# Optimization experiments

Hardware: AMD Instinct MI355X
Metric: run time of the kernel (lower is better)

Reference implementation:

```python
import jax, jax.numpy as jnp
import numpy as np

TOP_K = 6  # heapq.nlargest(6, ...) in the original

N_USERS_ROWS = 8192
EMB_DIM = 512
NUM_USER_IDS = 8192
NUM_ITEMS = 4096


def setup_inputs() -> dict:
    key = jax.random.key(0)
    k1, k2, k3, k4 = jax.random.split(key, 4)
    users_embeddings = jax.random.normal(k1, (N_USERS_ROWS, EMB_DIM), dtype=jnp.float32)
    n_users = jax.random.randint(k2, (N_USERS_ROWS,), 0, NUM_USER_IDS, dtype=jnp.int64)
    n_entitys = jax.random.randint(k3, (N_USERS_ROWS,), 0, NUM_ITEMS, dtype=jnp.int64)
    # 0/1 membership matrix standing in for the `course` dict: user_id -> set of items
    interactions = jax.random.randint(k4, (NUM_USER_IDS, NUM_ITEMS), 0, 2, dtype=jnp.int32)
    return {
        "users_embeddings": users_embeddings,
        "n_users": n_users,
        "n_entitys": n_entitys,
        "interactions": interactions,
    }


def reference(users_embeddings, n_users, n_entitys, interactions):
    # Pairwise cosine similarity: normalize rows, one GEMM.  [N, N]
    norms = jnp.linalg.norm(users_embeddings, axis=-1, keepdims=True)
    xn = users_embeddings / norms
    sim = jnp.einsum("nd,md->nm", xn, xn)
    # top-6 most similar users per row (includes self, like the original)
    top_vals, top_idx = jax.lax.top_k(sim, TOP_K)  # [N, 6] each
    # choice(course=n_entitys[l], user=n_users[idx]) -> 0/1 membership gather
    neighbor_user_ids = n_users[top_idx]            # [N, 6]
    memb = interactions[neighbor_user_ids, n_entitys[:, None]]  # [N, 6] int
    # p[l] = sum_k sim(l, idx_k) * memb / 6
    user_choice_degree = jnp.sum(top_vals * memb.astype(top_vals.dtype), axis=-1) / 6.0
    return user_choice_degree
```

## Files before the change

kernel.cpp:

```cpp
#include <hip/hip_runtime.h>
#include <math.h>

typedef unsigned char  uchar_t;
typedef unsigned int   uint32;
typedef __attribute__((ext_vector_type(4)))  int   i32x4;
typedef __attribute__((ext_vector_type(8)))  int   i32x8;
typedef __attribute__((ext_vector_type(16))) float f32x16;

#define EMB     512
#define NROWS   8192
#define NITEMS  4096
#define NSPLIT  16
#define CPS     512
#define CTILE   128
#define QTILE   128
#define NSTEPS  32
#define LDEPTH  8
#define KEEP    8
#define NRESC   16

#define GLOAD_LDS(gp, lp) __builtin_amdgcn_global_load_lds( \
    (const __attribute__((address_space(1))) void*)(gp),    \
    (__attribute__((address_space(3))) void*)(lp), 16, 0, 0)

__device__ inline uint32 packkey(float v, int idx) {
    uint32 u = __float_as_uint(v);
    uint32 s = u ^ ((u & 0x80000000u) ? 0xFFFFFFFFu : 0x80000000u);
    return (s & 0xFFFFE000u) | ((uint32)idx ^ 0x1FFFu);
}

__global__ void prep_kernel(const float* __restrict__ E,
                            uchar_t* __restrict__ Xq, double* __restrict__ invd) {
    const int row  = blockIdx.x * 4 + (threadIdx.x >> 6);
    const int lane = threadIdx.x & 63;
    const float4* p = (const float4*)(E + (size_t)row * EMB);
    float4 f0 = p[lane];
    float4 f1 = p[lane + 64];
    double s = (double)f0.x*f0.x + (double)f0.y*f0.y + (double)f0.z*f0.z + (double)f0.w*f0.w
             + (double)f1.x*f1.x + (double)f1.y*f1.y + (double)f1.z*f1.z + (double)f1.w*f1.w;
#pragma unroll
    for (int m = 32; m > 0; m >>= 1) s += __shfl_xor(s, m);
    const double inv = 1.0 / sqrt(s);
    if (lane == 0) invd[row] = inv;
    const float sc = (float)inv * 16.0f;
    int w0 = 0, w1 = 0;
    w0 = __builtin_amdgcn_cvt_pk_fp8_f32(f0.x * sc, f0.y * sc, w0, false);
    w0 = __builtin_amdgcn_cvt_pk_fp8_f32(f0.z * sc, f0.w * sc, w0, true);
    w1 = __builtin_amdgcn_cvt_pk_fp8_f32(f1.x * sc, f1.y * sc, w1, false);
    w1 = __builtin_amdgcn_cvt_pk_fp8_f32(f1.z * sc, f1.w * sc, w1, true);
    ((int2*)(Xq + (size_t)row * EMB))[lane] = make_int2(w0, w1);
}

__global__ __launch_bounds__(256, 4) void sim_topk_mfma(
    const uchar_t* __restrict__ Xq, uint32* __restrict__ keys_out) {

    __shared__ union {
        struct { uchar_t A[2][8192]; uchar_t B[2][8192]; } s;
        struct { uint32 mk[128][37]; } m;
    } sh;

    const int t     = threadIdx.x;
    const int lane  = t & 63;
    const int wave  = t >> 6;
    const int wm    = wave >> 1;
    const int wn    = wave & 1;
    const int rb    = blockIdx.x >> 4;
    const int split = blockIdx.x & 15;
    const int qbase = rb * QTILE;
    const int l31   = lane & 31;
    const int l5    = lane >> 5;

    const bool isA   = (wave < 2);
    const int  jb4   = (wave & 1) * 4;
    const int  mbase = isA ? split * CPS : qbase;
    const uchar_t* base =
        Xq + (size_t)(mbase + (jb4 >> 1) * 32 + l31) * EMB + (l5 << 4);
    const uchar_t* cur[4];
    cur[0] = base;
    cur[1] = base + 32;
    cur[2] = base + (size_t)32 * EMB;
    cur[3] = base + (size_t)32 * EMB + 32;

    auto stage = [&](int buf) {
        uchar_t* bp = (isA ? sh.s.A[buf] : sh.s.B[buf]) + jb4 * 1024;
        GLOAD_LDS(cur[0], bp);
        GLOAD_LDS(cur[1], bp + 1024);
        GLOAD_LDS(cur[2], bp + 2048);
        GLOAD_LDS(cur[3], bp + 3072);
    };

    uint32 tv[2][LDEPTH];
#pragma unroll
    for (int fc = 0; fc < 2; ++fc)
#pragma unroll
        for (int d = 0; d < LDEPTH; ++d) tv[fc][d] = 0u;

    f32x16 acc[2][2];
#pragma unroll
    for (int fr = 0; fr < 2; ++fr)
#pragma unroll
        for (int fc = 0; fc < 2; ++fc)
#pragma unroll
            for (int q = 0; q < 16; ++q) acc[fr][fc][q] = 0.f;

    stage(0);

    const int fo = (l5 << 10) + (l31 << 4);

    union U8 { i32x8 v8; struct { i32x4 lo; i32x4 hi; } h; };

#pragma unroll 1
    for (int s = 0; s < NSTEPS; ++s) {
        const int buf = s & 1;

        __syncthreads();

        if (s + 1 < NSTEPS) {
            const bool newct = ((s + 1) & 7) == 0;
            const long d = isA ? (newct ? (long)CTILE * EMB - 7 * 64 : 64)
                               : (newct ? -(long)(7 * 64) : 64);
#pragma unroll
            for (int c = 0; c < 4; ++c) cur[c] += d;
            stage((s + 1) & 1);
        }

        U8 a0, a1, b;
        {
            const int ca = (wm * 2) * 2048;
            a0.h.lo = *(const i32x4*)&sh.s.A[buf][ca + fo];
            a0.h.hi = *(const i32x4*)&sh.s.A[buf][ca + 512 + fo];
            a1.h.lo = *(const i32x4*)&sh.s.A[buf][ca + 2048 + fo];
            a1.h.hi = *(const i32x4*)&sh.s.A[buf][ca + 2048 + 512 + fo];
        }
        {
            const int cb = (wn * 2) * 2048;
            b.h.lo = *(const i32x4*)&sh.s.B[buf][cb + fo];
            b.h.hi = *(const i32x4*)&sh.s.B[buf][cb + 512 + fo];
        }
        acc[0][0] = __builtin_amdgcn_mfma_scale_f32_32x32x64_f8f6f4(
            a0.v8, b.v8, acc[0][0], 0, 0, 0, 0x7F7F7F7F, 0, 0x7F7F7F7F);
        acc[1][0] = __builtin_amdgcn_mfma_scale_f32_32x32x64_f8f6f4(
            a1.v8, b.v8, acc[1][0], 0, 0, 0, 0x7F7F7F7F, 0, 0x7F7F7F7F);
        {
            const int cb = (wn * 2 + 1) * 2048;
            b.h.lo = *(const i32x4*)&sh.s.B[buf][cb + fo];
            b.h.hi = *(const i32x4*)&sh.s.B[buf][cb + 512 + fo];
        }
        acc[0][1] = __builtin_amdgcn_mfma_scale_f32_32x32x64_f8f6f4(
            a0.v8, b.v8, acc[0][1], 0, 0, 0, 0x7F7F7F7F, 0, 0x7F7F7F7F);
        acc[1][1] = __builtin_amdgcn_mfma_scale_f32_32x32x64_f8f6f4(
            a1.v8, b.v8, acc[1][1], 0, 0, 0, 0x7F7F7F7F, 0, 0x7F7F7F7F);

        if ((s & 7) == 7) {
            const int cand0 = split * CPS + (s >> 3) * CTILE;
#pragma unroll
            for (int fc = 0; fc < 2; ++fc) {
#pragma unroll
                for (int fr = 0; fr < 2; ++fr) {
                    float t0 = fmaxf(fmaxf(acc[fr][fc][0],  acc[fr][fc][1]),  acc[fr][fc][2]);
                    float t1 = fmaxf(fmaxf(acc[fr][fc][3],  acc[fr][fc][4]),  acc[fr][fc][5]);
                    float t2 = fmaxf(fmaxf(acc[fr][fc][6],  acc[fr][fc][7]),  acc[fr][fc][8]);
                    float t3 = fmaxf(fmaxf(acc[fr][fc][9],  acc[fr][fc][10]), acc[fr][fc][11]);
                    float t4 = fmaxf(fmaxf(acc[fr][fc][12], acc[fr][fc][13]), acc[fr][fc][14]);
                    float mx = fmaxf(fmaxf(fmaxf(t0, t1), t2),
                                     fmaxf(fmaxf(t3, t4), acc[fr][fc][15]));
                    if (packkey(mx, 0) > tv[fc][LDEPTH - 1]) {
                        const int jb = cand0 + wm * 64 + fr * 32 + (l5 << 2);
#pragma unroll
                        for (int reg = 0; reg < 16; ++reg) {
                            const int ci = jb + (reg & 3) + ((reg >> 2) << 3);
                            uint32 key = packkey(acc[fr][fc][reg], ci);
                            if (key > tv[fc][LDEPTH - 1]) {
                                uint32 c2 = key;
#pragma unroll
                                for (int d = 0; d < LDEPTH; ++d) {
                                    const uint32 a  = tv[fc][d];
                                    const uint32 hi = a > c2 ? a : c2;
                                    c2              = a > c2 ? c2 : a;
                                    tv[fc][d] = hi;
                                }
                            }
                        }
                    }
#pragma unroll
                    for (int q = 0; q < 16; ++q) acc[fr][fc][q] = 0.f;
                }
            }
        }
    }

    __syncthreads();
#pragma unroll
    for (int fc = 0; fc < 2; ++fc) {
        const int col = wn * 64 + fc * 32 + l31;
        const int sl  = wm * 2 + l5;
#pragma unroll
        for (int d = 0; d < LDEPTH; ++d) sh.m.mk[col][sl * 9 + d] = tv[fc][d];
        sh.m.mk[col][sl * 9 + 8] = 0u;
    }
    __syncthreads();
    if (t < 128) {
        int p[4] = {0, 0, 0, 0};
        const size_t base2 = ((size_t)(qbase + t) * NSPLIT + split) * KEEP;
#pragma unroll 1
        for (int sel = 0; sel < KEEP; ++sel) {
            uint32 bk = 0; int bl = 0;
#pragma unroll
            for (int l = 0; l < 4; ++l) {
                uint32 k = sh.m.mk[t][l * 9 + p[l]];
                if (k > bk) { bk = k; bl = l; }
            }
            p[bl]++;
            keys_out[base2 + sel] = bk;
        }
    }
}

__global__ __launch_bounds__(256) void rescue_kernel(
    const float* __restrict__ E, const double* __restrict__ invd,
    const uint32* __restrict__ keys,
    const int* __restrict__ n_users, const int* __restrict__ n_entitys,
    const int* __restrict__ interactions, float* __restrict__ out) {

    __shared__ uint32 skeys[128];
    __shared__ float4 sq[128];
    __shared__ int    scand[NRESC];
    __shared__ double sd[NRESC];
    __shared__ int    sci[NRESC];
    __shared__ float  smemb[NRESC];
    __shared__ double contrib[8];

    const int t   = threadIdx.x;
    const int row = blockIdx.x;

    if (t < 128) {
        skeys[t] = keys[(size_t)row * 128 + t];
        sq[t]    = ((const float4*)(E + (size_t)row * EMB))[t];
    }
    if (t < NRESC) scand[t] = 0;
    if (t < 8)     contrib[t] = 0.0;
    __syncthreads();

    if (t < 128) {
        const uint32 k = skeys[t];
        int r = 0;
#pragma unroll 16
        for (int j = 0; j < 128; ++j) {
            const uint32 kj = skeys[j];
            r += (kj > k) || (kj == k && j < t);
        }
        if (r < NRESC) scand[r] = (int)((k & 0x1FFFu) ^ 0x1FFFu);
    }
    __syncthreads();

    const int g    = t >> 4;
    const int l16  = t & 15;
    const int cand = scand[g] & (NROWS - 1);
    const float4* C = (const float4*)(E + (size_t)cand * EMB);
    double acc = 0.0;
#pragma unroll
    for (int j = 0; j < 8; ++j) {
        float4 c = C[l16 + 16 * j];
        float4 q = sq[l16 + 16 * j];
        acc += (double)q.x * c.x + (double)q.y * c.y
             + (double)q.z * c.z + (double)q.w * c.w;
    }
#pragma unroll
    for (int m = 8; m >= 1; m >>= 1) acc += __shfl_xor(acc, m, 16);

    const int ent = n_entitys[row];
    if (l16 == 0) { sd[g] = acc * invd[row] * invd[cand]; sci[g] = cand; }
    if (l16 == 1) {
        const int uid = n_users[cand];
        smemb[g] = (float)interactions[(size_t)uid * NITEMS + ent];
    }
    __syncthreads();

    if (t < NRESC) {
        const double v  = sd[t];
        const int    ci = sci[t];
        int r = 0;
#pragma unroll
        for (int j = 0; j < NRESC; ++j) {
            const double vj = sd[j];
            const int    cj = sci[j];
            r += (vj > v) || (vj == v && (cj < ci || (cj == ci && j < t)));
        }
        if (r < 6) contrib[r] = v * (double)smemb[t];
    }
    __syncthreads();
    if (t == 0) {
        const double sum = contrib[0] + contrib[1] + contrib[2]
                         + contrib[3] + contrib[4] + contrib[5];
        out[row] = (float)(sum * (1.0 / 6.0));
    }
}

extern "C" void kernel_launch(void* const* d_in, const int* in_sizes, int n_in,
                              void* d_out, int out_size, void* d_ws, size_t ws_size,
                              hipStream_t stream) {
    const float* E            = (const float*)d_in[0];
    const int*   n_users      = (const int*)d_in[1];
    const int*   n_entitys    = (const int*)d_in[2];
    const int*   interactions = (const int*)d_in[3];
    float*       out          = (float*)d_out;

    uchar_t* Xq   = (uchar_t*)d_ws;
    double*  invd = (double*)(Xq + (size_t)NROWS * EMB);
    uint32*  keys = (uint32*)(invd + NROWS);

    prep_kernel<<<NROWS / 4, 256, 0, stream>>>(E, Xq, invd);
    sim_topk_mfma<<<(NROWS / QTILE) * NSPLIT, 256, 0, stream>>>(Xq, keys);
    rescue_kernel<<<NROWS, 256, 0, stream>>>(E, invd, keys, n_users, n_entitys,
                                             interactions, out);
}
```

Baseline: 331.1 us.

## Load MFMA operands directly from global memory, dropping LDS double buffering

The similarity kernel stops staging the A and B fp8 tiles into shared memory with global_load_lds. Each wave now reads its own MFMA operand fragments straight from global memory into registers across an unrolled 8-step K loop. This removes the per-step __syncthreads and LDS traffic, and shared memory is left holding only the merge buffer. In exchange, operand rows shared by two waves are fetched twice, which leans on the L1/L2 caches. Lanes also make strided per-row 32-byte reads, and the K permutation changes, though it stays the same for both operands.

```diff
diff --git a/kernel.cpp b/kernel.cpp
--- a/kernel.cpp
+++ b/kernel.cpp
@@ -14,14 +14,10 @@
 #define CPS     512
 #define CTILE   128
 #define QTILE   128
-#define NSTEPS  32
+#define NCT     4
 #define LDEPTH  8
 #define KEEP    8
 #define NRESC   16
-
-#define GLOAD_LDS(gp, lp) __builtin_amdgcn_global_load_lds( \
-    (const __attribute__((address_space(1))) void*)(gp),    \
-    (__attribute__((address_space(3))) void*)(lp), 16, 0, 0)
 
 __device__ inline uint32 packkey(float v, int idx) {
     uint32 u = __float_as_uint(v);
@@ -54,10 +50,7 @@
 __global__ __launch_bounds__(256, 4) void sim_topk_mfma(
     const uchar_t* __restrict__ Xq, uint32* __restrict__ keys_out) {
 
-    __shared__ union {
-        struct { uchar_t A[2][8192]; uchar_t B[2][8192]; } s;
-        struct { uint32 mk[128][37]; } m;
-    } sh;
+    __shared__ uint32 mk[128][37];
 
     const int t     = threadIdx.x;
     const int lane  = t & 63;
@@ -70,24 +63,10 @@
     const int l31   = lane & 31;
     const int l5    = lane >> 5;
 
-    const bool isA   = (wave < 2);
-    const int  jb4   = (wave & 1) * 4;
-    const int  mbase = isA ? split * CPS : qbase;
-    const uchar_t* base =
-        Xq + (size_t)(mbase + (jb4 >> 1) * 32 + l31) * EMB + (l5 << 4);
-    const uchar_t* cur[4];
-    cur[0] = base;
-    cur[1] = base + 32;
-    cur[2] = base + (size_t)32 * EMB;
-    cur[3] = base + (size_t)32 * EMB + 32;
-
-    auto stage = [&](int buf) {
-        uchar_t* bp = (isA ? sh.s.A[buf] : sh.s.B[buf]) + jb4 * 1024;
-        GLOAD_LDS(cur[0], bp);
-        GLOAD_LDS(cur[1], bp + 1024);
-        GLOAD_LDS(cur[2], bp + 2048);
-        GLOAD_LDS(cur[3], bp + 3072);
-    };
+    const uchar_t* pa0 = Xq + (size_t)(split * CPS + wm * 64 + l31) * EMB + (l5 << 5);
+    const uchar_t* pa1 = pa0 + (size_t)32 * EMB;
+    const uchar_t* pb0 = Xq + (size_t)(qbase + wn * 64 + l31) * EMB + (l5 << 5);
+    const uchar_t* pb1 = pb0 + (size_t)32 * EMB;
 
     uint32 tv[2][LDEPTH];
 #pragma unroll
@@ -103,100 +82,78 @@
 #pragma unroll
             for (int q = 0; q < 16; ++q) acc[fr][fc][q] = 0.f;
 
-    stage(0);
-
-    const int fo = (l5 << 10) + (l31 << 4);
-
     union U8 { i32x8 v8; struct { i32x4 lo; i32x4 hi; } h; };
 
 #pragma unroll 1
-    for (int s = 0; s < NSTEPS; ++s) {
-        const int buf = s & 1;
-
-        __syncthreads();
-
-        if (s + 1 < NSTEPS) {
-            const bool newct = ((s + 1) & 7) == 0;
-            const long d = isA ? (newct ? (long)CTILE * EMB - 7 * 64 : 64)
-                               : (newct ? -(long)(7 * 64) : 64);
-#pragma unroll
-            for (int c = 0; c < 4; ++c) cur[c] += d;
-            stage((s + 1) & 1);
-        }
-
-        U8 a0, a1, b;
-        {
-            const int ca = (wm * 2) * 2048;
-            a0.h.lo = *(const i32x4*)&sh.s.A[buf][ca + fo];
-            a0.h.hi = *(const i32x4*)&sh.s.A[buf][ca + 512 + fo];
-            a1.h.lo = *(const i32x4*)&sh.s.A[buf][ca + 2048 + fo];
-            a1.h.hi = *(const i32x4*)&sh.s.A[buf][ca + 2048 + 512 + fo];
-        }
-        {
-            const int cb = (wn * 2) * 2048;
-            b.h.lo = *(const i32x4*)&sh.s.B[buf][cb + fo];
-            b.h.hi = *(const i32x4*)&sh.s.B[buf][cb + 512 + fo];
-        }
-        acc[0][0] = __builtin_amdgcn_mfma_scale_f32_32x32x64_f8f6f4(
-            a0.v8, b.v8, acc[0][0], 0, 0, 0, 0x7F7F7F7F, 0, 0x7F7F7F7F);
-        acc[1][0] = __builtin_amdgcn_mfma_scale_f32_32x32x64_f8f6f4(
-            a1.v8, b.v8, acc[1][0], 0, 0, 0, 0x7F7F7F7F, 0, 0x7F7F7F7F);
-        {
-            const int cb = (wn * 2 + 1) * 2048;
-            b.h.lo = *(const i32x4*)&sh.s.B[buf][cb + fo];
-            b.h.hi = *(const i32x4*)&sh.s.B[buf][cb + 512 + fo];
-        }
-        acc[0][1] = __builtin_amdgcn_mfma_scale_f32_32x32x64_f8f6f4(
-            a0.v8, b.v8, acc[0][1], 0, 0, 0, 0x7F7F7F7F, 0, 0x7F7F7F7F);
-        acc[1][1] = __builtin_amdgcn_mfma_scale_f32_32x32x64_f8f6f4(
-            a1.v8, b.v8, acc[1][1], 0, 0, 0, 0x7F7F7F7F, 0, 0x7F7F7F7F);
-
-        if ((s & 7) == 7) {
-            const int cand0 = split * CPS + (s >> 3) * CTILE;
-#pragma unroll
-            for (int fc = 0; fc < 2; ++fc) {
-#pragma unroll
-                for (int fr = 0; fr < 2; ++fr) {
-                    float t0 = fmaxf(fmaxf(acc[fr][fc][0],  acc[fr][fc][1]),  acc[fr][fc][2]);
-                    float t1 = fmaxf(fmaxf(acc[fr][fc][3],  acc[fr][fc][4]),  acc[fr][fc][5]);
-                    float t2 = fmaxf(fmaxf(acc[fr][fc][6],  acc[fr][fc][7]),  acc[fr][fc][8]);
-                    float t3 = fmaxf(fmaxf(acc[fr][fc][9],  acc[fr][fc][10]), acc[fr][fc][11]);
-                    float t4 = fmaxf(fmaxf(acc[fr][fc][12], acc[fr][fc][13]), acc[fr][fc][14]);
-                    float mx = fmaxf(fmaxf(fmaxf(t0, t1), t2),
-                                     fmaxf(fmaxf(t3, t4), acc[fr][fc][15]));
-                    if (packkey(mx, 0) > tv[fc][LDEPTH - 1]) {
-                        const int jb = cand0 + wm * 64 + fr * 32 + (l5 << 2);
-#pragma unroll
-                        for (int reg = 0; reg < 16; ++reg) {
-                            const int ci = jb + (reg & 3) + ((reg >> 2) << 3);
-                            uint32 key = packkey(acc[fr][fc][reg], ci);
-                            if (key > tv[fc][LDEPTH - 1]) {
-                                uint32 c2 = key;
-#pragma unroll
-                                for (int d = 0; d < LDEPTH; ++d) {
-                                    const uint32 a  = tv[fc][d];
-                                    const uint32 hi = a > c2 ? a : c2;
-                                    c2              = a > c2 ? c2 : a;
-                                    tv[fc][d] = hi;
-                                }
+    for (int ct = 0; ct < NCT; ++ct) {
+#pragma unroll
+        for (int ks = 0; ks < 8; ++ks) {
+            const int ko = ks * 64;
+            U8 a0, a1, b0, b1;
+            a0.h.lo = *(const i32x4*)(pa0 + ko);
+            a0.h.hi = *(const i32x4*)(pa0 + ko + 16);
+            a1.h.lo = *(const i32x4*)(pa1 + ko);
+            a1.h.hi = *(const i32x4*)(pa1 + ko + 16);
+            b0.h.lo = *(const i32x4*)(pb0 + ko);
+            b0.h.hi = *(const i32x4*)(pb0 + ko + 16);
+            b1.h.lo = *(const i32x4*)(pb1 + ko);
+            b1.h.hi = *(const i32x4*)(pb1 + ko + 16);
+            acc[0][0] = __builtin_amdgcn_mfma_scale_f32_32x32x64_f8f6f4(
+                a0.v8, b0.v8, acc[0][0], 0, 0, 0, 0x7F7F7F7F, 0, 0x7F7F7F7F);
+            acc[1][0] = __builtin_amdgcn_mfma_scale_f32_32x32x64_f8f6f4(
+                a1.v8, b0.v8, acc[1][0], 0, 0, 0, 0x7F7F7F7F, 0, 0x7F7F7F7F);
+            acc[0][1] = __builtin_amdgcn_mfma_scale_f32_32x32x64_f8f6f4(
+                a0.v8, b1.v8, acc[0][1], 0, 0, 0, 0x7F7F7F7F, 0, 0x7F7F7F7F);
+            acc[1][1] = __builtin_amdgcn_mfma_scale_f32_32x32x64_f8f6f4(
+                a1.v8, b1.v8, acc[1][1], 0, 0, 0, 0x7F7F7F7F, 0, 0x7F7F7F7F);
+        }
+
+        const int cand0 = split * CPS + ct * CTILE;
+#pragma unroll
+        for (int fc = 0; fc < 2; ++fc) {
+#pragma unroll
+            for (int fr = 0; fr < 2; ++fr) {
+                float t0 = fmaxf(fmaxf(acc[fr][fc][0],  acc[fr][fc][1]),  acc[fr][fc][2]);
+                float t1 = fmaxf(fmaxf(acc[fr][fc][3],  acc[fr][fc][4]),  acc[fr][fc][5]);
+                float t2 = fmaxf(fmaxf(acc[fr][fc][6],  acc[fr][fc][7]),  acc[fr][fc][8]);
+                float t3 = fmaxf(fmaxf(acc[fr][fc][9],  acc[fr][fc][10]), acc[fr][fc][11]);
+                float t4 = fmaxf(fmaxf(acc[fr][fc][12], acc[fr][fc][13]), acc[fr][fc][14]);
+                float mx = fmaxf(fmaxf(fmaxf(t0, t1), t2),
+                                 fmaxf(fmaxf(t3, t4), acc[fr][fc][15]));
+                if (packkey(mx, 0) > tv[fc][LDEPTH - 1]) {
+                    const int jb = cand0 + wm * 64 + fr * 32 + (l5 << 2);
+#pragma unroll
+                    for (int reg = 0; reg < 16; ++reg) {
+                        const int ci = jb + (reg & 3) + ((reg >> 2) << 3);
+                        uint32 key = packkey(acc[fr][fc][reg], ci);
+                        if (key > tv[fc][LDEPTH - 1]) {
+                            uint32 c2 = key;
+#pragma unroll
+                            for (int d = 0; d < LDEPTH; ++d) {
+                                const uint32 a  = tv[fc][d];
+                                const uint32 hi = a > c2 ? a : c2;
+                                c2              = a > c2 ? c2 : a;
+                                tv[fc][d] = hi;
                             }
                         }
                     }
-#pragma unroll
-                    for (int q = 0; q < 16; ++q) acc[fr][fc][q] = 0.f;
                 }
+#pragma unroll
+                for (int q = 0; q < 16; ++q) acc[fr][fc][q] = 0.f;
             }
         }
-    }
-
-    __syncthreads();
+
+        pa0 += (size_t)CTILE * EMB;
+        pa1 += (size_t)CTILE * EMB;
+    }
+
 #pragma unroll
     for (int fc = 0; fc < 2; ++fc) {
         const int col = wn * 64 + fc * 32 + l31;
         const int sl  = wm * 2 + l5;
 #pragma unroll
-        for (int d = 0; d < LDEPTH; ++d) sh.m.mk[col][sl * 9 + d] = tv[fc][d];
-        sh.m.mk[col][sl * 9 + 8] = 0u;
+        for (int d = 0; d < LDEPTH; ++d) mk[col][sl * 9 + d] = tv[fc][d];
+        mk[col][sl * 9 + 8] = 0u;
     }
     __syncthreads();
     if (t < 128) {
@@ -207,7 +164,7 @@
             uint32 bk = 0; int bl = 0;
 #pragma unroll
             for (int l = 0; l < 4; ++l) {
-                uint32 k = sh.m.mk[t][l * 9 + p[l]];
+                uint32 k = mk[t][l * 9 + p[l]];
                 if (k > bk) { bk = k; bl = l; }
             }
             p[bl]++;
```

Measured after the change: 461.0 us. 39.2% more time.

## Pre-swizzle FP8 embeddings into MFMA tile layout to avoid LDS bank conflicts

Applied to the files above, without the earlier changes.

The quantize kernel now writes FP8 rows in a blocked layout (32-row groups by 64-byte k-slices, interleaved in 8-byte chunks), so each GEMM k-step loads a contiguous 2KB block per group. The GEMM reads LDS with 8-byte loads at a 256-byte stride instead of 16-byte loads at a 1024-byte stride, which is intended to cut LDS bank conflicts and simplify the global-to-LDS staging addresses. Both B fragments are loaded up front, which uses more registers. The merge loop also replaces the dynamic p[bl]++ with a predicated update so p stays in registers.

```diff
diff --git a/kernel.cpp b/kernel.cpp
--- a/kernel.cpp
+++ b/kernel.cpp
@@ -3,7 +3,7 @@
 
 typedef unsigned char  uchar_t;
 typedef unsigned int   uint32;
-typedef __attribute__((ext_vector_type(4)))  int   i32x4;
+typedef __attribute__((ext_vector_type(2)))  int   i32x2;
 typedef __attribute__((ext_vector_type(8)))  int   i32x8;
 typedef __attribute__((ext_vector_type(16))) float f32x16;
 
@@ -48,7 +48,9 @@
     w0 = __builtin_amdgcn_cvt_pk_fp8_f32(f0.z * sc, f0.w * sc, w0, true);
     w1 = __builtin_amdgcn_cvt_pk_fp8_f32(f1.x * sc, f1.y * sc, w1, false);
     w1 = __builtin_amdgcn_cvt_pk_fp8_f32(f1.z * sc, f1.w * sc, w1, true);
-    ((int2*)(Xq + (size_t)row * EMB))[lane] = make_int2(w0, w1);
+    const int g  = row >> 5, l = row & 31;
+    const int ks = lane >> 3, j8 = lane & 7;
+    *(int2*)(Xq + ((size_t)(g * 8 + ks)) * 2048 + j8 * 256 + l * 8) = make_int2(w0, w1);
 }
 
 __global__ __launch_bounds__(256, 4) void sim_topk_mfma(
@@ -70,23 +72,22 @@
     const int l31   = lane & 31;
     const int l5    = lane >> 5;
 
-    const bool isA   = (wave < 2);
-    const int  jb4   = (wave & 1) * 4;
-    const int  mbase = isA ? split * CPS : qbase;
-    const uchar_t* base =
-        Xq + (size_t)(mbase + (jb4 >> 1) * 32 + l31) * EMB + (l5 << 4);
+    const bool isA = (wave < 2);
+    const int  wj  = wave & 1;
+    const int  g0  = (isA ? split * CPS : qbase) >> 5;
     const uchar_t* cur[4];
-    cur[0] = base;
-    cur[1] = base + 32;
-    cur[2] = base + (size_t)32 * EMB;
-    cur[3] = base + (size_t)32 * EMB + 32;
+#pragma unroll
+    for (int c = 0; c < 4; ++c) {
+        const int g = g0 + wj * 2 + (c >> 1);
+        cur[c] = Xq + ((size_t)g * 8) * 2048 + (c & 1) * 1024 + lane * 16;
+    }
+    const long incA_ct = (long)4 * 8 * 2048 - 7 * 2048;
+    const long incB_ct = -(long)(7 * 2048);
 
     auto stage = [&](int buf) {
-        uchar_t* bp = (isA ? sh.s.A[buf] : sh.s.B[buf]) + jb4 * 1024;
-        GLOAD_LDS(cur[0], bp);
-        GLOAD_LDS(cur[1], bp + 1024);
-        GLOAD_LDS(cur[2], bp + 2048);
-        GLOAD_LDS(cur[3], bp + 3072);
+        uchar_t* bp = (isA ? sh.s.A[buf] : sh.s.B[buf]) + wj * 4096;
+#pragma unroll
+        for (int c = 0; c < 4; ++c) GLOAD_LDS(cur[c], bp + c * 1024);
     };
 
     uint32 tv[2][LDEPTH];
@@ -105,9 +106,9 @@
 
     stage(0);
 
-    const int fo = (l5 << 10) + (l31 << 4);
-
-    union U8 { i32x8 v8; struct { i32x4 lo; i32x4 hi; } h; };
+    const int fo = (l5 << 10) + (l31 << 3);
+
+    union U8 { i32x8 v8; i32x2 q[4]; };
 
 #pragma unroll 1
     for (int s = 0; s < NSTEPS; ++s) {
@@ -117,39 +118,34 @@
 
         if (s + 1 < NSTEPS) {
             const bool newct = ((s + 1) & 7) == 0;
-            const long d = isA ? (newct ? (long)CTILE * EMB - 7 * 64 : 64)
-                               : (newct ? -(long)(7 * 64) : 64);
+            const long d = isA ? (newct ? incA_ct : 2048)
+                               : (newct ? incB_ct : 2048);
 #pragma unroll
             for (int c = 0; c < 4; ++c) cur[c] += d;
             stage((s + 1) & 1);
         }
 
-        U8 a0, a1, b;
+        U8 a0, a1, b0, b1;
         {
-            const int ca = (wm * 2) * 2048;
-            a0.h.lo = *(const i32x4*)&sh.s.A[buf][ca + fo];
-            a0.h.hi = *(const i32x4*)&sh.s.A[buf][ca + 512 + fo];
-            a1.h.lo = *(const i32x4*)&sh.s.A[buf][ca + 2048 + fo];
-            a1.h.hi = *(const i32x4*)&sh.s.A[buf][ca + 2048 + 512 + fo];
-        }
-        {
-            const int cb = (wn * 2) * 2048;
-            b.h.lo = *(const i32x4*)&sh.s.B[buf][cb + fo];
-            b.h.hi = *(const i32x4*)&sh.s.B[buf][cb + 512 + fo];
-        }
+            const uchar_t* Ab = sh.s.A[buf] + (wm * 4096) + fo;
+            const uchar_t* Bb = sh.s.B[buf] + (wn * 4096) + fo;
+#pragma unroll
+            for (int jj = 0; jj < 4; ++jj) {
+                a0.q[jj] = *(const i32x2*)(Ab + jj * 256);
+                a1.q[jj] = *(const i32x2*)(Ab + 2048 + jj * 256);
+                b0.q[jj] = *(const i32x2*)(Bb + jj * 256);
+                b1.q[jj] = *(const i32x2*)(Bb + 2048 + jj * 256);
+            }
+        }
+
         acc[0][0] = __builtin_amdgcn_mfma_scale_f32_32x32x64_f8f6f4(
-            a0.v8, b.v8, acc[0][0], 0, 0, 0, 0x7F7F7F7F, 0, 0x7F7F7F7F);
+            a0.v8, b0.v8, acc[0][0], 0, 0, 0, 0x7F7F7F7F, 0, 0x7F7F7F7F);
         acc[1][0] = __builtin_amdgcn_mfma_scale_f32_32x32x64_f8f6f4(
-            a1.v8, b.v8, acc[1][0], 0, 0, 0, 0x7F7F7F7F, 0, 0x7F7F7F7F);
-        {
-            const int cb = (wn * 2 + 1) * 2048;
-            b.h.lo = *(const i32x4*)&sh.s.B[buf][cb + fo];
-            b.h.hi = *(const i32x4*)&sh.s.B[buf][cb + 512 + fo];
-        }
+            a1.v8, b0.v8, acc[1][0], 0, 0, 0, 0x7F7F7F7F, 0, 0x7F7F7F7F);
         acc[0][1] = __builtin_amdgcn_mfma_scale_f32_32x32x64_f8f6f4(
-            a0.v8, b.v8, acc[0][1], 0, 0, 0, 0x7F7F7F7F, 0, 0x7F7F7F7F);
+            a0.v8, b1.v8, acc[0][1], 0, 0, 0, 0x7F7F7F7F, 0, 0x7F7F7F7F);
         acc[1][1] = __builtin_amdgcn_mfma_scale_f32_32x32x64_f8f6f4(
-            a1.v8, b.v8, acc[1][1], 0, 0, 0, 0x7F7F7F7F, 0, 0x7F7F7F7F);
+            a1.v8, b1.v8, acc[1][1], 0, 0, 0, 0x7F7F7F7F, 0, 0x7F7F7F7F);
 
         if ((s & 7) == 7) {
             const int cand0 = split * CPS + (s >> 3) * CTILE;
@@ -210,7 +206,8 @@
                 uint32 k = sh.m.mk[t][l * 9 + p[l]];
                 if (k > bk) { bk = k; bl = l; }
             }
-            p[bl]++;
+#pragma unroll
+            for (int l = 0; l < 4; ++l) p[l] += (bl == l);
             keys_out[base2 + sel] = bk;
         }
     }
```

Measured after the change: 317.2 us. 1.04x faster.
